# Optimization experiments

Measured on AMD Instinct MI355X. Metric: run time of the kernel, lower is better.

The kernel has to match this reference:

```python
import jax, jax.numpy as jnp
import numpy as np

N, C, D = 4096, 256, 128
CURV = 1.0  # c; ball curvature is -c


def setup_inputs() -> dict:
    key = jax.random.key(0)
    k1, k2, k3 = jax.random.split(key, 3)
    # points inside the unit ball (norm < 1): scale randn by 0.05
    output_before = 0.05 * jax.random.normal(k1, (N, D), dtype=jnp.float32)
    a_mlr = jax.random.uniform(k2, (C, D), minval=-0.05, maxval=0.05, dtype=jnp.float32)
    p_mlr = jax.random.uniform(k3, (C, D), minval=-0.05, maxval=0.05, dtype=jnp.float32)
    return {"output_before": output_before, "a_mlr": a_mlr, "p_mlr": p_mlr}


def _hyp_mlr(output_before, a_mlr, p_mlr):
    c = CURV
    x = output_before[:, None, :]          # [N,1,D]
    mp = -p_mlr[None, :, :]                # [1,C,D]  (-p)
    xy = jnp.sum(mp * x, axis=-1)          # [N,C]  <-p, x>
    p2 = jnp.sum(mp * mp, axis=-1)         # [1,C]  ||p||^2
    x2 = jnp.sum(x * x, axis=-1)           # [N,1]  ||x||^2
    # Mobius addition (-p) (+) x on the Poincare ball with curvature -c
    num_p = (1.0 + 2.0 * c * xy + c * x2)[..., None] * mp
    num_x = (1.0 - c * p2)[..., None] * x
    den = (1.0 + 2.0 * c * xy + (c * c) * p2 * x2)[..., None]
    res = (num_p + num_x) / den            # [N,C,D]
    # conformal factor lambda = 2 / (1 - ||res||^2)
    lam = 2.0 / (1.0 - jnp.sum(res * res, axis=-1))   # [N,C]
    norm_a = jnp.linalg.norm(a_mlr, axis=-1)          # [C]
    a_hat = a_mlr / jnp.maximum(norm_a, 1e-12)[:, None]
    dot = jnp.sum(res * a_hat[None, :, :], axis=-1)   # [N,C]
    return 2.0 * norm_a[None, :] * jnp.arcsinh(dot * lam)  # [N,C]


def reference(output_before, a_mlr, p_mlr):
    return _hyp_mlr(output_before, a_mlr, p_mlr)
```

## Files before the change

### kernel.cpp

```cpp
#include <hip/hip_runtime.h>
#include <hip/hip_bf16.h>

typedef __attribute__((ext_vector_type(4))) float  f32x4;
typedef __attribute__((ext_vector_type(8))) float  f32x8;
typedef __attribute__((ext_vector_type(8))) __bf16 bf16x8;

#define NR 4096
#define NC 256
#define DD 128
#define BR 64
#define BC 32
#define CURVC 1.0f

__global__ __launch_bounds__(256) void hyp_mlr_kernel(
    const float* __restrict__ Xg,
    const float* __restrict__ Ag,
    const float* __restrict__ Pg,
    float* __restrict__ Out)
{
    __shared__ f32x4  ldsX[BR * 32];
    __shared__ bf16x8 ldsP[BC * 16];
    __shared__ bf16x8 ldsA[BC * 16];
    __shared__ float  scrC[3][4][BC];
    __shared__ float  scrR[2][BR];
    __shared__ float  colP2[BC], colMPA[BC], colINA[BC], colNA[BC];
    __shared__ float  rowX2[BR];

    const int t    = threadIdx.x;
    const int row0 = blockIdx.x * BR;
    const int c0   = blockIdx.y * BC;

    #pragma unroll
    for (int q = 0; q < 8; ++q) {
        int uid = q * 256 + t;
        int row = uid >> 5, u = uid & 31;
        ldsX[row * 32 + (u ^ (row & 7))] =
            *(const f32x4*)(Xg + (size_t)(row0 + row) * DD + u * 4);
    }
    #pragma unroll
    for (int q = 0; q < 2; ++q) {
        int uid = q * 256 + t;
        int row = uid >> 4, u = uid & 15;
        f32x8 pf = *(const f32x8*)(Pg + (size_t)(c0 + row) * DD + u * 8);
        f32x8 af = *(const f32x8*)(Ag + (size_t)(c0 + row) * DD + u * 8);
        bf16x8 pv, av;
        #pragma unroll
        for (int e = 0; e < 8; ++e) { pv[e] = (__bf16)pf[e]; av[e] = (__bf16)af[e]; }
        ldsP[row * 16 + (u ^ (row & 7))] = pv;
        ldsA[row * 16 + (u ^ (row & 7))] = av;
    }
    __syncthreads();

    if (t < 128) {
        int c = t & 31, q = t >> 5;
        float sp2 = 0.f, spa = 0.f, sa2 = 0.f;
        #pragma unroll
        for (int uu = 0; uu < 4; ++uu) {
            int u = q * 4 + uu;
            bf16x8 pv = ldsP[c * 16 + (u ^ (c & 7))];
            bf16x8 av = ldsA[c * 16 + (u ^ (c & 7))];
            #pragma unroll
            for (int e = 0; e < 8; ++e) {
                float pe = (float)pv[e], ae = (float)av[e];
                sp2 += pe * pe; spa += pe * ae; sa2 += ae * ae;
            }
        }
        scrC[0][q][c] = sp2; scrC[1][q][c] = spa; scrC[2][q][c] = sa2;
    } else {
        int r = (t - 128) >> 1, h = t & 1;
        float sx2 = 0.f;
        #pragma unroll
        for (int uu = 0; uu < 16; ++uu) {
            int u = h * 16 + uu;
            f32x4 xv = ldsX[r * 32 + (u ^ (r & 7))];
            sx2 += xv[0]*xv[0] + xv[1]*xv[1] + xv[2]*xv[2] + xv[3]*xv[3];
        }
        scrR[h][r] = sx2;
    }
    __syncthreads();

    if (t < 32) {
        float p2 = scrC[0][0][t] + scrC[0][1][t] + scrC[0][2][t] + scrC[0][3][t];
        float pa = scrC[1][0][t] + scrC[1][1][t] + scrC[1][2][t] + scrC[1][3][t];
        float a2 = scrC[2][0][t] + scrC[2][1][t] + scrC[2][2][t] + scrC[2][3][t];
        float na  = sqrtf(a2);
        float ina = 1.0f / fmaxf(na, 1e-12f);
        colP2[t] = p2; colNA[t] = na; colINA[t] = ina;
        colMPA[t] = -pa * ina;
    } else if (t >= 32 && t < 96) {
        int r = t - 32;
        rowX2[r] = scrR[0][r] + scrR[1][r];
    }
    __syncthreads();

    const int rb = t & 15;
    const int cb = t >> 4;
    float accP[4][2] = {{0.f,0.f},{0.f,0.f},{0.f,0.f},{0.f,0.f}};
    float accA[4][2] = {{0.f,0.f},{0.f,0.f},{0.f,0.f},{0.f,0.f}};

    for (int kc = 0; kc < 16; ++kc) {
        float xv[4][8];
        #pragma unroll
        for (int i = 0; i < 4; ++i) {
            int r = rb + 16 * i;
            f32x4 x0 = ldsX[r * 32 + ((2 * kc)     ^ (r & 7))];
            f32x4 x1 = ldsX[r * 32 + ((2 * kc + 1) ^ (r & 7))];
            xv[i][0] = x0[0]; xv[i][1] = x0[1]; xv[i][2] = x0[2]; xv[i][3] = x0[3];
            xv[i][4] = x1[0]; xv[i][5] = x1[1]; xv[i][6] = x1[2]; xv[i][7] = x1[3];
        }
        float pv[2][8], av[2][8];
        #pragma unroll
        for (int j = 0; j < 2; ++j) {
            int c = cb + 16 * j;
            bf16x8 p8 = ldsP[c * 16 + (kc ^ (c & 7))];
            bf16x8 a8 = ldsA[c * 16 + (kc ^ (c & 7))];
            #pragma unroll
            for (int e = 0; e < 8; ++e) { pv[j][e] = (float)p8[e]; av[j][e] = (float)a8[e]; }
        }
        #pragma unroll
        for (int i = 0; i < 4; ++i)
            #pragma unroll
            for (int j = 0; j < 2; ++j)
                #pragma unroll
                for (int e = 0; e < 8; ++e) {
                    accP[i][j] += xv[i][e] * pv[j][e];
                    accA[i][j] += xv[i][e] * av[j][e];
                }
    }

    #pragma unroll
    for (int i = 0; i < 4; ++i) {
        int   r  = rb + 16 * i;
        float x2 = rowX2[r];
        #pragma unroll
        for (int j = 0; j < 2; ++j) {
            int   c   = cb + 16 * j;
            float xy  = -accP[i][j];
            float xa  = accA[i][j] * colINA[c];
            float p2  = colP2[c];
            float A1  = 1.f + 2.f * CURVC * xy + CURVC * x2;
            float B1  = 1.f - CURVC * p2;
            float den = 1.f + 2.f * CURVC * xy + CURVC * CURVC * p2 * x2;
            float idn = 1.f / den;
            float r2  = (A1 * A1 * p2 + 2.f * A1 * B1 * xy + B1 * B1 * x2) * idn * idn;
            float lam = 2.f / (1.f - r2);
            float z   = (A1 * colMPA[c] + B1 * xa) * idn * lam;
            float az  = fabsf(z);
            float as  = logf(az + sqrtf(az * az + 1.f));
            float o   = 2.f * colNA[c] * copysignf(as, z);
            Out[(size_t)(row0 + r) * NC + (c0 + c)] = o;
        }
    }
}

extern "C" void kernel_launch(void* const* d_in, const int* in_sizes, int n_in,
                              void* d_out, int out_size, void* d_ws, size_t ws_size,
                              hipStream_t stream) {
    const float* X = (const float*)d_in[0];
    const float* A = (const float*)d_in[1];
    const float* P = (const float*)d_in[2];
    float* out = (float*)d_out;
    dim3 grid(NR / BR, NC / BC);
    hipLaunchKernelGGL(hyp_mlr_kernel, grid, dim3(256), 0, stream, X, A, P, out);
}
```

Baseline: 70.87 us.

## Compute dot products with bf16 MFMA and fuse norm reductions into loads

Replaces the scalar FP32 FMA inner product loop with MFMA 16x16x32 bf16 instructions, and stores X in LDS as bf16 instead of fp32. Row and column norms are now computed during the global loads using wave shuffles, which removes two barriers and the scratch buffers. logf is swapped for the fast __logf. The cost is bf16 rounding of X in the dot products, which adds error on top of the existing bf16 P and A.

```diff
diff --git a/kernel.cpp b/kernel.cpp
--- a/kernel.cpp
+++ b/kernel.cpp
@@ -4,6 +4,7 @@
 typedef __attribute__((ext_vector_type(4))) float  f32x4;
 typedef __attribute__((ext_vector_type(8))) float  f32x8;
 typedef __attribute__((ext_vector_type(8))) __bf16 bf16x8;
+typedef __attribute__((ext_vector_type(4))) __bf16 bf16x4;
 
 #define NR 4096
 #define NC 256
@@ -18,125 +19,110 @@
     const float* __restrict__ Pg,
     float* __restrict__ Out)
 {
-    __shared__ f32x4  ldsX[BR * 32];
+    __shared__ bf16x8 ldsX[BR * 16];
     __shared__ bf16x8 ldsP[BC * 16];
     __shared__ bf16x8 ldsA[BC * 16];
-    __shared__ float  scrC[3][4][BC];
-    __shared__ float  scrR[2][BR];
+    __shared__ float  rowX2[BR];
     __shared__ float  colP2[BC], colMPA[BC], colINA[BC], colNA[BC];
-    __shared__ float  rowX2[BR];
 
     const int t    = threadIdx.x;
     const int row0 = blockIdx.x * BR;
     const int c0   = blockIdx.y * BC;
 
     #pragma unroll
-    for (int q = 0; q < 8; ++q) {
+    for (int q = 0; q < 4; ++q) {
         int uid = q * 256 + t;
-        int row = uid >> 5, u = uid & 31;
-        ldsX[row * 32 + (u ^ (row & 7))] =
-            *(const f32x4*)(Xg + (size_t)(row0 + row) * DD + u * 4);
+        int row = uid >> 4, u = uid & 15;
+        f32x8 xf = *(const f32x8*)(Xg + (size_t)(row0 + row) * DD + u * 8);
+        bf16x8 xv;
+        float s = 0.f;
+        #pragma unroll
+        for (int e = 0; e < 8; ++e) { xv[e] = (__bf16)xf[e]; s += xf[e] * xf[e]; }
+        ldsX[row * 16 + (u ^ (row & 7))] = xv;
+        #pragma unroll
+        for (int m = 1; m < 16; m <<= 1) s += __shfl_xor(s, m);
+        if ((t & 15) == 0) rowX2[row] = s;
     }
     #pragma unroll
     for (int q = 0; q < 2; ++q) {
         int uid = q * 256 + t;
-        int row = uid >> 4, u = uid & 15;
-        f32x8 pf = *(const f32x8*)(Pg + (size_t)(c0 + row) * DD + u * 8);
-        f32x8 af = *(const f32x8*)(Ag + (size_t)(c0 + row) * DD + u * 8);
+        int col = uid >> 4, u = uid & 15;
+        f32x8 pf = *(const f32x8*)(Pg + (size_t)(c0 + col) * DD + u * 8);
+        f32x8 af = *(const f32x8*)(Ag + (size_t)(c0 + col) * DD + u * 8);
         bf16x8 pv, av;
+        float sp2 = 0.f, spa = 0.f, sa2 = 0.f;
         #pragma unroll
-        for (int e = 0; e < 8; ++e) { pv[e] = (__bf16)pf[e]; av[e] = (__bf16)af[e]; }
-        ldsP[row * 16 + (u ^ (row & 7))] = pv;
-        ldsA[row * 16 + (u ^ (row & 7))] = av;
+        for (int e = 0; e < 8; ++e) {
+            float pe = pf[e], ae = af[e];
+            pv[e] = (__bf16)pe; av[e] = (__bf16)ae;
+            sp2 += pe * pe; spa += pe * ae; sa2 += ae * ae;
+        }
+        ldsP[col * 16 + (u ^ (col & 7))] = pv;
+        ldsA[col * 16 + (u ^ (col & 7))] = av;
+        #pragma unroll
+        for (int m = 1; m < 16; m <<= 1) {
+            sp2 += __shfl_xor(sp2, m);
+            spa += __shfl_xor(spa, m);
+            sa2 += __shfl_xor(sa2, m);
+        }
+        if ((t & 15) == 0) {
+            float na  = sqrtf(sa2);
+            float ina = 1.f / fmaxf(na, 1e-12f);
+            colP2[col] = sp2; colNA[col] = na; colINA[col] = ina;
+            colMPA[col] = -spa * ina;
+        }
     }
     __syncthreads();
 
-    if (t < 128) {
-        int c = t & 31, q = t >> 5;
-        float sp2 = 0.f, spa = 0.f, sa2 = 0.f;
-        #pragma unroll
-        for (int uu = 0; uu < 4; ++uu) {
-            int u = q * 4 + uu;
-            bf16x8 pv = ldsP[c * 16 + (u ^ (c & 7))];
-            bf16x8 av = ldsA[c * 16 + (u ^ (c & 7))];
-            #pragma unroll
-            for (int e = 0; e < 8; ++e) {
-                float pe = (float)pv[e], ae = (float)av[e];
-                sp2 += pe * pe; spa += pe * ae; sa2 += ae * ae;
-            }
-        }
-        scrC[0][q][c] = sp2; scrC[1][q][c] = spa; scrC[2][q][c] = sa2;
-    } else {
-        int r = (t - 128) >> 1, h = t & 1;
-        float sx2 = 0.f;
-        #pragma unroll
-        for (int uu = 0; uu < 16; ++uu) {
-            int u = h * 16 + uu;
-            f32x4 xv = ldsX[r * 32 + (u ^ (r & 7))];
-            sx2 += xv[0]*xv[0] + xv[1]*xv[1] + xv[2]*xv[2] + xv[3]*xv[3];
-        }
-        scrR[h][r] = sx2;
-    }
-    __syncthreads();
+    const int l  = t & 63, w = t >> 6;
+    const int lo = l & 15, hi = l >> 4;
+    const __bf16* xb = (const __bf16*)ldsX;
+    const __bf16* pb = (const __bf16*)ldsP;
+    const __bf16* ab = (const __bf16*)ldsA;
 
-    if (t < 32) {
-        float p2 = scrC[0][0][t] + scrC[0][1][t] + scrC[0][2][t] + scrC[0][3][t];
-        float pa = scrC[1][0][t] + scrC[1][1][t] + scrC[1][2][t] + scrC[1][3][t];
-        float a2 = scrC[2][0][t] + scrC[2][1][t] + scrC[2][2][t] + scrC[2][3][t];
-        float na  = sqrtf(a2);
-        float ina = 1.0f / fmaxf(na, 1e-12f);
-        colP2[t] = p2; colNA[t] = na; colINA[t] = ina;
-        colMPA[t] = -pa * ina;
-    } else if (t >= 32 && t < 96) {
-        int r = t - 32;
-        rowX2[r] = scrR[0][r] + scrR[1][r];
-    }
-    __syncthreads();
+    const int xrow = 16 * w + lo;
+    const int xsw  = xrow & 7;
+    const int hsel = 4 * (hi & 1);
+    const int uq   = hi >> 1;
 
-    const int rb = t & 15;
-    const int cb = t >> 4;
-    float accP[4][2] = {{0.f,0.f},{0.f,0.f},{0.f,0.f},{0.f,0.f}};
-    float accA[4][2] = {{0.f,0.f},{0.f,0.f},{0.f,0.f},{0.f,0.f}};
+    f32x4 zv = {0.f, 0.f, 0.f, 0.f};
+    f32x4 accP[2] = {zv, zv};
+    f32x4 accA[2] = {zv, zv};
 
-    for (int kc = 0; kc < 16; ++kc) {
-        float xv[4][8];
-        #pragma unroll
-        for (int i = 0; i < 4; ++i) {
-            int r = rb + 16 * i;
-            f32x4 x0 = ldsX[r * 32 + ((2 * kc)     ^ (r & 7))];
-            f32x4 x1 = ldsX[r * 32 + ((2 * kc + 1) ^ (r & 7))];
-            xv[i][0] = x0[0]; xv[i][1] = x0[1]; xv[i][2] = x0[2]; xv[i][3] = x0[3];
-            xv[i][4] = x1[0]; xv[i][5] = x1[1]; xv[i][6] = x1[2]; xv[i][7] = x1[3];
-        }
-        float pv[2][8], av[2][8];
+    #pragma unroll
+    for (int kk = 0; kk < 4; ++kk) {
+        int u0 = 4 * kk + uq;
+        bf16x4 h0 = *(const bf16x4*)(xb + xrow * 128 + ((u0    ) ^ xsw) * 8 + hsel);
+        bf16x4 h1 = *(const bf16x4*)(xb + xrow * 128 + ((u0 + 2) ^ xsw) * 8 + hsel);
+        bf16x8 xf;
+        xf[0]=h0[0]; xf[1]=h0[1]; xf[2]=h0[2]; xf[3]=h0[3];
+        xf[4]=h1[0]; xf[5]=h1[1]; xf[6]=h1[2]; xf[7]=h1[3];
         #pragma unroll
         for (int j = 0; j < 2; ++j) {
-            int c = cb + 16 * j;
-            bf16x8 p8 = ldsP[c * 16 + (kc ^ (c & 7))];
-            bf16x8 a8 = ldsA[c * 16 + (kc ^ (c & 7))];
-            #pragma unroll
-            for (int e = 0; e < 8; ++e) { pv[j][e] = (float)p8[e]; av[j][e] = (float)a8[e]; }
+            int pc = 16 * j + lo, sw = pc & 7;
+            bf16x4 p0 = *(const bf16x4*)(pb + pc * 128 + ((u0    ) ^ sw) * 8 + hsel);
+            bf16x4 p1 = *(const bf16x4*)(pb + pc * 128 + ((u0 + 2) ^ sw) * 8 + hsel);
+            bf16x4 a0 = *(const bf16x4*)(ab + pc * 128 + ((u0    ) ^ sw) * 8 + hsel);
+            bf16x4 a1 = *(const bf16x4*)(ab + pc * 128 + ((u0 + 2) ^ sw) * 8 + hsel);
+            bf16x8 pfr, afr;
+            pfr[0]=p0[0]; pfr[1]=p0[1]; pfr[2]=p0[2]; pfr[3]=p0[3];
+            pfr[4]=p1[0]; pfr[5]=p1[1]; pfr[6]=p1[2]; pfr[7]=p1[3];
+            afr[0]=a0[0]; afr[1]=a0[1]; afr[2]=a0[2]; afr[3]=a0[3];
+            afr[4]=a1[0]; afr[5]=a1[1]; afr[6]=a1[2]; afr[7]=a1[3];
+            accP[j] = __builtin_amdgcn_mfma_f32_16x16x32_bf16(xf, pfr, accP[j], 0, 0, 0);
+            accA[j] = __builtin_amdgcn_mfma_f32_16x16x32_bf16(xf, afr, accA[j], 0, 0, 0);
         }
-        #pragma unroll
-        for (int i = 0; i < 4; ++i)
-            #pragma unroll
-            for (int j = 0; j < 2; ++j)
-                #pragma unroll
-                for (int e = 0; e < 8; ++e) {
-                    accP[i][j] += xv[i][e] * pv[j][e];
-                    accA[i][j] += xv[i][e] * av[j][e];
-                }
     }
 
     #pragma unroll
-    for (int i = 0; i < 4; ++i) {
-        int   r  = rb + 16 * i;
-        float x2 = rowX2[r];
+    for (int r = 0; r < 4; ++r) {
+        int   rr = 16 * w + 4 * hi + r;
+        float x2 = rowX2[rr];
         #pragma unroll
         for (int j = 0; j < 2; ++j) {
-            int   c   = cb + 16 * j;
-            float xy  = -accP[i][j];
-            float xa  = accA[i][j] * colINA[c];
+            int   c   = 16 * j + lo;
+            float xy  = -accP[j][r];
+            float xa  = accA[j][r] * colINA[c];
             float p2  = colP2[c];
             float A1  = 1.f + 2.f * CURVC * xy + CURVC * x2;
             float B1  = 1.f - CURVC * p2;
@@ -146,9 +132,9 @@
             float lam = 2.f / (1.f - r2);
             float z   = (A1 * colMPA[c] + B1 * xa) * idn * lam;
             float az  = fabsf(z);
-            float as  = logf(az + sqrtf(az * az + 1.f));
+            float as  = __logf(az + sqrtf(az * az + 1.f));
             float o   = 2.f * colNA[c] * copysignf(as, z);
-            Out[(size_t)(row0 + r) * NC + (c0 + c)] = o;
+            Out[(size_t)(row0 + rr) * NC + (c0 + c)] = o;
         }
     }
 }
```

After: 63.67 us. 1.11x faster.
